# Optimization experiments

Hardware: AMD Instinct MI355X
Metric: run time of the kernel (lower is better)

Reference implementation:

```python
import jax, jax.numpy as jnp
from jax import lax
import numpy as np

B = 8192   # samples
L = 32     # predicted chars per sample (num_chars[i])
M = 32     # target labels per sample (num_labels[i])
C = 96     # character classes


def _edit_trace(pred, tgt):
    """Levenshtein DP + backtrace for one sample.
    pred: [L] int, tgt: [M] int.
    Returns (ti, tj, valid) of length L+M: 1-based (i,j) positions of the
    diagonal (match/substitute) moves on the optimal edit path, as emitted by
    distance_and_trace; valid masks non-diagonal / out-of-path steps."""
    Ls, Ms = pred.shape[0], tgt.shape[0]
    cost = (pred[:, None] != tgt[None, :]).astype(jnp.int32)  # [L,M]
    row0 = jnp.arange(Ms + 1, dtype=jnp.int32)

    def row_step(prev, crow):
        first = prev[0] + 1
        def col_step(left, z):
            up, diag, c = z
            v = jnp.minimum(jnp.minimum(up + 1, left + 1), diag + c)
            return v, v
        _, rest = lax.scan(col_step, first, (prev[1:], prev[:-1], crow))
        new = jnp.concatenate([first[None], rest])
        return new, new

    _, rows = lax.scan(row_step, row0, cost)
    D = jnp.concatenate([row0[None, :], rows], axis=0)  # [L+1, M+1]

    def bt_step(carry, _):
        i, j = carry
        c = cost[jnp.maximum(i - 1, 0), jnp.maximum(j - 1, 0)]
        dij = D[i, j]
        diag = (i > 0) & (j > 0) & (D[i - 1, j - 1] + c == dij)
        up = (~diag) & (i > 0) & (D[i - 1, j] + 1 == dij)
        left = (~diag) & (~up) & (j > 0)
        ni = i - (diag | up).astype(jnp.int32)
        nj = j - (diag | left).astype(jnp.int32)
        return (ni, nj), (i, j, diag)

    (_, _), (ti, tj, valid) = lax.scan(
        bt_step, (jnp.int32(Ls), jnp.int32(Ms)), None, length=Ls + Ms)
    return ti, tj, valid


def _forward(x, y, num_chars, num_labels):
    b = num_chars.shape[0]
    c = x.shape[1]
    l = x.shape[0] // b
    m = y.shape[0] // b
    logits = x.reshape(b, l, c)          # [B,L,C]
    labels = y.reshape(b, m)             # [B,M]
    pred = jnp.argmax(logits, axis=-1)   # torch.max(x,1) indices
    ti, tj, valid = jax.vmap(_edit_trace)(pred, labels)  # [B, L+M] each
    logp = jax.nn.log_softmax(logits, axis=-1)
    xi = jnp.where(valid, ti - 1, 0)     # trace[:,0]-1 (+ per-sample offset via reshape)
    yi = jnp.where(valid, tj - 1, 0)     # trace[:,1]-1
    lab = jnp.take_along_axis(labels, yi, axis=1)                 # [B,L+M]
    lp = jnp.take_along_axis(logp, xi[..., None], axis=1)         # [B,L+M,C]
    ce = -jnp.take_along_axis(lp, lab[..., None], axis=2)[..., 0]  # [B,L+M]
    cnt = valid.sum(axis=1)
    per_sample = jnp.where(valid, ce, 0.0).sum(axis=1) / jnp.maximum(cnt, 1)
    nonempty = cnt > 0                   # attenuation: skip empty traces
    total = jnp.where(nonempty, per_sample, 0.0).sum()
    return total / nonempty.sum()


def setup_inputs() -> dict:
    key = jax.random.key(0)
    k1, k2 = jax.random.split(key)
    x = jax.random.normal(k1, (B * L, C), dtype=jnp.float32)
    y = jax.random.randint(k2, (B * M,), 0, C, dtype=jnp.int32)
    num_chars = jnp.full((B,), L, dtype=jnp.int32)
    num_labels = jnp.full((B,), M, dtype=jnp.int32)
    return {"x": x, "y": y, "num_chars": num_chars, "num_labels": num_labels}


def reference(x, y, num_chars, num_labels):
    return _forward(x, y, num_chars, num_labels)
```

## Files before the change

kernel.cpp:

```cpp
#include <hip/hip_runtime.h>
#include <stdint.h>

#define BNUM  8192
#define LROWS 32
#define MLAB  32
#define CCLS  96
#define WPB   4
#define SPW   2
#define SPB   (WPB*SPW)
#define NBLK  (BNUM/SPB)

__global__ __launch_bounds__(256, 4) void editloss_main(
    const float* __restrict__ x, const int* __restrict__ y,
    float* __restrict__ partial_sum, float* __restrict__ partial_cnt)
{
    __shared__ float  ceTab[SPB][LROWS * MLAB];
    __shared__ float2 lpS[SPB][LROWS];
    __shared__ float  psum[SPB];
    __shared__ float  pcnt[SPB];

    const int w    = threadIdx.x >> 6;
    const int lane = threadIdx.x & 63;
    const int g    = lane >> 5;
    const int u    = lane & 31;
    const int s    = w * SPW + g;
    const int sb   = blockIdx.x * SPB + s;

    const float* xs    = x + (size_t)sb * (LROWS * CCLS);
    const int    lab_u = y[sb * MLAB + u];

    {
        const float4* rowv = (const float4*)(xs + (size_t)u * CCLS);
        float bmax[4]; int bidx[4]; float bsum[4];
#pragma unroll
        for (int c = 0; c < 4; ++c) { bmax[c] = -1e30f; bidx[c] = 0; bsum[c] = 0.f; }
#pragma unroll
        for (int c = 0; c < 4; ++c) {
#pragma unroll
            for (int k = 0; k < 6; ++k) {
                const float4 v = rowv[c * 6 + k];
                const int base = (c * 6 + k) * 4;
                if (v.x > bmax[c]) { bmax[c] = v.x; bidx[c] = base + 0; }
                if (v.y > bmax[c]) { bmax[c] = v.y; bidx[c] = base + 1; }
                if (v.z > bmax[c]) { bmax[c] = v.z; bidx[c] = base + 2; }
                if (v.w > bmax[c]) { bmax[c] = v.w; bidx[c] = base + 3; }
                bsum[c] += __expf(v.x) + __expf(v.y) + __expf(v.z) + __expf(v.w);
            }
        }
        float m = bmax[0]; int idx = bidx[0];
#pragma unroll
        for (int c = 1; c < 4; ++c)
            if (bmax[c] > m) { m = bmax[c]; idx = bidx[c]; }
        const float lse = __logf((bsum[0] + bsum[1]) + (bsum[2] + bsum[3]));
        lpS[s][u] = make_float2(lse, (float)idx);
    }
    asm volatile("s_waitcnt lgkmcnt(0)" ::: "memory");

    {
        const float* gcol = xs + lab_u;
#pragma unroll
        for (int r = 0; r < LROWS; ++r) {
            const float2 lp = lpS[s][r];
            const float  xg = gcol[r * CCLS];
            const float  ce = lp.x - xg;
            ceTab[s][r * MLAB + u] = ((int)lp.y == lab_u) ? ce : -ce;
        }
    }
    asm volatile("s_waitcnt lgkmcnt(0)" ::: "memory");

    const int j = u + 1;
    int   prevW = 0;   float prevCE = 0.f;
    int   diagW = 0;   float diagCE = 0.f;
#pragma unroll 4
    for (int d = 1; d <= LROWS + MLAB; ++d) {
        const int   lWs  = __shfl_up(prevW, 1);
        const float lCEs = __shfl_up(prevCE, 1);
        const int i = d - j;
        const int   lW  = (u == 0) ? max(i, 0)     : lWs;
        const float lCE = (u == 0) ? 0.f           : lCEs;
        const int   dW  = (u == 0) ? max(i - 1, 0) : diagW;
        const float dCE = (u == 0) ? 0.f           : diagCE;
        int curW; float curCE;
        if (i <= 0) {
            curW = j; curCE = 0.f;
        } else if (i > LROWS) {
            curW = prevW; curCE = prevCE;
        } else {
            const int uD = prevW & 255, uC = prevW >> 8;
            const int lD = lW & 255,    lC = lW >> 8;
            const int dD = dW & 255,    dC = dW >> 8;
            const float ct  = ceTab[s][(i - 1) * MLAB + u];
            const int   c   = (ct < 0.f) ? 1 : 0;
            const int nD = min(min(uD, lD) + 1, dD + c);
            const bool dg = (dD + c == nD);
            const bool up = !dg && (uD + 1 == nD);
            int nC; float nCE;
            if (dg)      { nC = dC + 1; nCE = dCE + fabsf(ct); }
            else if (up) { nC = uC;     nCE = prevCE;          }
            else         { nC = lC;     nCE = lCE;             }
            curW = nD | (nC << 8);
            curCE = nCE;
        }
        diagW = lWs; diagCE = lCEs;
        prevW = curW; prevCE = curCE;
    }

    if (u == 31) {
        const int cnt = prevW >> 8;
        psum[s] = (cnt > 0) ? prevCE / (float)cnt : 0.f;
        pcnt[s] = (cnt > 0) ? 1.f : 0.f;
    }
    __syncthreads();
    if (threadIdx.x == 0) {
        float ss = 0.f, cc = 0.f;
#pragma unroll
        for (int k = 0; k < SPB; ++k) { ss += psum[k]; cc += pcnt[k]; }
        partial_sum[blockIdx.x] = ss;
        partial_cnt[blockIdx.x] = cc;
    }
}

__global__ __launch_bounds__(256) void editloss_finalize(
    const float* __restrict__ partial_sum, const float* __restrict__ partial_cnt,
    float* __restrict__ out, int nblocks)
{
    float s = 0.f, c = 0.f;
    for (int k = threadIdx.x; k < nblocks; k += 256) {
        s += partial_sum[k];
        c += partial_cnt[k];
    }
#pragma unroll
    for (int d = 32; d >= 1; d >>= 1) {
        s += __shfl_xor(s, d);
        c += __shfl_xor(c, d);
    }
    __shared__ float ss[4], cc[4];
    const int w = threadIdx.x >> 6, lane = threadIdx.x & 63;
    if (lane == 0) { ss[w] = s; cc[w] = c; }
    __syncthreads();
    if (threadIdx.x == 0) {
        const float S  = ss[0] + ss[1] + ss[2] + ss[3];
        const float C2 = cc[0] + cc[1] + cc[2] + cc[3];
        out[0] = (C2 > 0.f) ? (S / C2) : 0.f;
    }
}

extern "C" void kernel_launch(void* const* d_in, const int* in_sizes, int n_in,
                              void* d_out, int out_size, void* d_ws, size_t ws_size,
                              hipStream_t stream) {
    const float* x = (const float*)d_in[0];
    const int*   y = (const int*)d_in[1];
    float* out = (float*)d_out;

    float* partial_sum = (float*)d_ws;
    float* partial_cnt = partial_sum + NBLK;

    editloss_main<<<NBLK, 256, 0, stream>>>(x, y, partial_sum, partial_cnt);
    editloss_finalize<<<1, 256, 0, stream>>>(partial_sum, partial_cnt, out, NBLK);
}
```

Before: 170.3 us.

## Fuse CE gather into wavefront DP, use DPP row shifts, batch logit loads

Removes the shared-memory ceTab precompute pass. The cross-entropy term is computed inline inside the anti-diagonal DP loop, reading the per-row logsumexp/argmax from LDS and gathering the label logit from global memory each step. The lane-to-lane shuffles become DPP wave_shr:1 operations, and the logit row loads are issued in two batches of 12 float4 to raise memory-level parallelism. In exchange it adds a clamped global gather on every DP iteration (including inactive ones), uses more registers, and relies on the DPP row-shift semantics within 32-lane halves.

```diff
diff --git a/kernel.cpp b/kernel.cpp
--- a/kernel.cpp
+++ b/kernel.cpp
@@ -10,11 +10,18 @@
 #define SPB   (WPB*SPW)
 #define NBLK  (BNUM/SPB)
 
+__device__ __forceinline__ int dpp_wshr1_i32(int v) {
+    return __builtin_amdgcn_update_dpp(0, v, 0x138, 0xF, 0xF, true);
+}
+__device__ __forceinline__ float dpp_wshr1_f32(float v) {
+    return __int_as_float(
+        __builtin_amdgcn_update_dpp(0, __float_as_int(v), 0x138, 0xF, 0xF, true));
+}
+
 __global__ __launch_bounds__(256, 4) void editloss_main(
     const float* __restrict__ x, const int* __restrict__ y,
     float* __restrict__ partial_sum, float* __restrict__ partial_cnt)
 {
-    __shared__ float  ceTab[SPB][LROWS * MLAB];
     __shared__ float2 lpS[SPB][LROWS];
     __shared__ float  psum[SPB];
     __shared__ float  pcnt[SPB];
@@ -34,18 +41,34 @@
         float bmax[4]; int bidx[4]; float bsum[4];
 #pragma unroll
         for (int c = 0; c < 4; ++c) { bmax[c] = -1e30f; bidx[c] = 0; bsum[c] = 0.f; }
+
+        float4 va[12];
 #pragma unroll
-        for (int c = 0; c < 4; ++c) {
+        for (int t = 0; t < 12; ++t) va[t] = rowv[t];
 #pragma unroll
-            for (int k = 0; k < 6; ++k) {
-                const float4 v = rowv[c * 6 + k];
-                const int base = (c * 6 + k) * 4;
-                if (v.x > bmax[c]) { bmax[c] = v.x; bidx[c] = base + 0; }
-                if (v.y > bmax[c]) { bmax[c] = v.y; bidx[c] = base + 1; }
-                if (v.z > bmax[c]) { bmax[c] = v.z; bidx[c] = base + 2; }
-                if (v.w > bmax[c]) { bmax[c] = v.w; bidx[c] = base + 3; }
-                bsum[c] += __expf(v.x) + __expf(v.y) + __expf(v.z) + __expf(v.w);
-            }
+        for (int t = 0; t < 12; ++t) {
+            const int c = t / 6;
+            const float4 v = va[t];
+            const int base = t * 4;
+            if (v.x > bmax[c]) { bmax[c] = v.x; bidx[c] = base + 0; }
+            if (v.y > bmax[c]) { bmax[c] = v.y; bidx[c] = base + 1; }
+            if (v.z > bmax[c]) { bmax[c] = v.z; bidx[c] = base + 2; }
+            if (v.w > bmax[c]) { bmax[c] = v.w; bidx[c] = base + 3; }
+            bsum[c] += __expf(v.x) + __expf(v.y) + __expf(v.z) + __expf(v.w);
+        }
+        float4 vb[12];
+#pragma unroll
+        for (int t = 0; t < 12; ++t) vb[t] = rowv[12 + t];
+#pragma unroll
+        for (int t = 0; t < 12; ++t) {
+            const int c = 2 + t / 6;
+            const float4 v = vb[t];
+            const int base = (12 + t) * 4;
+            if (v.x > bmax[c]) { bmax[c] = v.x; bidx[c] = base + 0; }
+            if (v.y > bmax[c]) { bmax[c] = v.y; bidx[c] = base + 1; }
+            if (v.z > bmax[c]) { bmax[c] = v.z; bidx[c] = base + 2; }
+            if (v.w > bmax[c]) { bmax[c] = v.w; bidx[c] = base + 3; }
+            bsum[c] += __expf(v.x) + __expf(v.y) + __expf(v.z) + __expf(v.w);
         }
         float m = bmax[0]; int idx = bidx[0];
 #pragma unroll
@@ -56,26 +79,20 @@
     }
     asm volatile("s_waitcnt lgkmcnt(0)" ::: "memory");
 
-    {
-        const float* gcol = xs + lab_u;
-#pragma unroll
-        for (int r = 0; r < LROWS; ++r) {
-            const float2 lp = lpS[s][r];
-            const float  xg = gcol[r * CCLS];
-            const float  ce = lp.x - xg;
-            ceTab[s][r * MLAB + u] = ((int)lp.y == lab_u) ? ce : -ce;
-        }
-    }
-    asm volatile("s_waitcnt lgkmcnt(0)" ::: "memory");
-
-    const int j = u + 1;
+    const int     j     = u + 1;
+    const float   fl    = (float)lab_u;
+    const float*  gcol  = xs + lab_u;
+    const float2* lpRow = lpS[s];
     int   prevW = 0;   float prevCE = 0.f;
     int   diagW = 0;   float diagCE = 0.f;
-#pragma unroll 4
+#pragma unroll 8
     for (int d = 1; d <= LROWS + MLAB; ++d) {
-        const int   lWs  = __shfl_up(prevW, 1);
-        const float lCEs = __shfl_up(prevCE, 1);
-        const int i = d - j;
+        const int   lWs  = dpp_wshr1_i32(prevW);
+        const float lCEs = dpp_wshr1_f32(prevCE);
+        const int i  = d - j;
+        const int ic = min(max(i - 1, 0), LROWS - 1);
+        const float2 lp = lpRow[ic];
+        const float  xg = gcol[ic * CCLS];
         const int   lW  = (u == 0) ? max(i, 0)     : lWs;
         const float lCE = (u == 0) ? 0.f           : lCEs;
         const int   dW  = (u == 0) ? max(i - 1, 0) : diagW;
@@ -89,15 +106,15 @@
             const int uD = prevW & 255, uC = prevW >> 8;
             const int lD = lW & 255,    lC = lW >> 8;
             const int dD = dW & 255,    dC = dW >> 8;
-            const float ct  = ceTab[s][(i - 1) * MLAB + u];
-            const int   c   = (ct < 0.f) ? 1 : 0;
+            const float ce = lp.x - xg;
+            const int   c  = (lp.y != fl) ? 1 : 0;
             const int nD = min(min(uD, lD) + 1, dD + c);
             const bool dg = (dD + c == nD);
             const bool up = !dg && (uD + 1 == nD);
             int nC; float nCE;
-            if (dg)      { nC = dC + 1; nCE = dCE + fabsf(ct); }
-            else if (up) { nC = uC;     nCE = prevCE;          }
-            else         { nC = lC;     nCE = lCE;             }
+            if (dg)      { nC = dC + 1; nCE = dCE + ce; }
+            else if (up) { nC = uC;     nCE = prevCE;   }
+            else         { nC = lC;     nCE = lCE;      }
             curW = nD | (nC << 8);
             curCE = nCE;
         }
```

Measured after the change: 227.6 us. +33.6%, slower.
